# Kernel tuning notes

Hardware: AMD Instinct MI355X
Metric: run time of the kernel (lower is better)

## Reference

```python
import jax, jax.numpy as jnp
import numpy as np

D = 64        # emb_size
L = 4         # n_layers
ND = 4        # directions per layer: v2c, c2v, v2k, k2v
N_VAR, N_CONS, N_CUT = 100000, 50000, 20000
E_VC, E_VK = 800000, 200000
EF = 8        # edge feature dim
LN_EPS = 1e-3  # keras LayerNormalization default epsilon


def mlp2(x, w1, b1, w2, b2):
    # Dense(relu) -> Dense(linear); dropout is identity (training=False)
    return jax.nn.relu(x @ w1 + b1) @ w2 + b2


def layer_norm(x, g, b):
    m = jnp.mean(x, axis=-1, keepdims=True)
    v = jnp.var(x, axis=-1, keepdims=True)
    return (x - m) * jax.lax.rsqrt(v + LN_EPS) * g + b


def message_pass(node, neigh, src, dst, ew, P, i):
    """One MessagePassingLayer. P is a tuple of stacked [16,...] params, i the layer index."""
    (mw1, mb1, mw2, mb2, gw, gb, uw1, ub1, uw2, ub2, lg, lb) = P
    msg = mlp2(neigh, mw1[i], mb1[i], mw2[i], mb2[i])          # [N_src, D]
    wm = msg[src] * ew                                          # [E, D] gather + weight
    n = node.shape[0]
    agg = jax.ops.segment_sum(wm, dst, num_segments=n)          # scatter_nd sum
    deg = jax.ops.segment_sum(ew, dst, num_segments=n)          # [n, 1]
    agg = agg / jnp.maximum(deg, 1.0)
    comb = jnp.concatenate([agg, node], axis=-1)                # [n, 2D]
    gate = jax.nn.sigmoid(comb @ gw[i] + gb[i])
    upd = mlp2(comb, uw1[i], ub1[i], uw2[i], ub2[i])
    out = gate * upd + (1.0 - gate) * node
    return layer_norm(out, lg[i], lb[i])


def edge_weight(src_f, dst_f, e_f, w1, b1, w2, b2):
    comb = jnp.concatenate([src_f, dst_f, e_f], axis=-1)
    return jax.nn.sigmoid(jax.nn.relu(comb @ w1 + b1) @ w2 + b2)  # [E, 1]


def setup_inputs() -> dict:
    keys = iter(jax.random.split(jax.random.key(0), 64))

    def p(shape, scale=0.05):
        return jax.random.normal(next(keys), shape, dtype=jnp.float32) * scale

    inp = {
        'variable_features': jax.random.normal(next(keys), (N_VAR, 19), dtype=jnp.float32),
        'constraint_features': jax.random.normal(next(keys), (N_CONS, 5), dtype=jnp.float32),
        'cut_features': jax.random.normal(next(keys), (N_CUT, 30), dtype=jnp.float32),
        'var_cons_edge_features': jax.random.normal(next(keys), (E_VC, EF), dtype=jnp.float32),
        'var_cut_edge_features': jax.random.normal(next(keys), (E_VK, EF), dtype=jnp.float32),
        'var_cons_edges': jnp.stack([
            jax.random.randint(next(keys), (E_VC,), 0, N_VAR, dtype=jnp.int32),
            jax.random.randint(next(keys), (E_VC,), 0, N_CONS, dtype=jnp.int32)]),
        'var_cut_edges': jnp.stack([
            jax.random.randint(next(keys), (E_VK,), 0, N_VAR, dtype=jnp.int32),
            jax.random.randint(next(keys), (E_VK,), 0, N_CUT, dtype=jnp.int32)]),
    }
    # embedding MLPs
    for name, din in [('var', 19), ('cons', 5), ('cut', 30)]:
        inp[f'{name}_w1'] = p((din, D)); inp[f'{name}_b1'] = p((D,))
        inp[f'{name}_w2'] = p((D, D));  inp[f'{name}_b2'] = p((D,))
    # edge weight modules (input 2D + edge_feat)
    for name in ['ewvc', 'ewvk']:
        inp[f'{name}_w1'] = p((2 * D + EF, D)); inp[f'{name}_b1'] = p((D,))
        inp[f'{name}_w2'] = p((D, 1));          inp[f'{name}_b2'] = p((1,))
    # 16 message passing layers, stacked; index = layer*4 + direction(v2c,c2v,v2k,k2v)
    NL = L * ND
    inp['mp_msg_w1'] = p((NL, D, D));  inp['mp_msg_b1'] = p((NL, D))
    inp['mp_msg_w2'] = p((NL, D, D));  inp['mp_msg_b2'] = p((NL, D))
    inp['mp_gate_w'] = p((NL, 2 * D, D)); inp['mp_gate_b'] = p((NL, D))
    inp['mp_upd_w1'] = p((NL, 2 * D, D)); inp['mp_upd_b1'] = p((NL, D))
    inp['mp_upd_w2'] = p((NL, D, D));  inp['mp_upd_b2'] = p((NL, D))
    inp['mp_ln_g'] = jnp.ones((NL, D), dtype=jnp.float32)
    inp['mp_ln_b'] = jnp.zeros((NL, D), dtype=jnp.float32)
    return inp


def reference(variable_features, constraint_features, cut_features,
              var_cons_edge_features, var_cut_edge_features,
              var_w1, var_b1, var_w2, var_b2,
              cons_w1, cons_b1, cons_w2, cons_b2,
              cut_w1, cut_b1, cut_w2, cut_b2,
              ewvc_w1, ewvc_b1, ewvc_w2, ewvc_b2,
              ewvk_w1, ewvk_b1, ewvk_w2, ewvk_b2,
              mp_msg_w1, mp_msg_b1, mp_msg_w2, mp_msg_b2,
              mp_gate_w, mp_gate_b, mp_upd_w1, mp_upd_b1,
              mp_upd_w2, mp_upd_b2, mp_ln_g, mp_ln_b,
              var_cons_edges, var_cut_edges):
    h_var = mlp2(variable_features, var_w1, var_b1, var_w2, var_b2)
    h_cons = mlp2(constraint_features, cons_w1, cons_b1, cons_w2, cons_b2)
    h_cut = mlp2(cut_features, cut_w1, cut_b1, cut_w2, cut_b2)

    vc_s, vc_d = var_cons_edges[0], var_cons_edges[1]
    vk_s, vk_d = var_cut_edges[0], var_cut_edges[1]

    vc_w = edge_weight(h_var[vc_s], h_cons[vc_d], var_cons_edge_features,
                       ewvc_w1, ewvc_b1, ewvc_w2, ewvc_b2)
    vk_w = edge_weight(h_var[vk_s], h_cut[vk_d], var_cut_edge_features,
                       ewvk_w1, ewvk_b1, ewvk_w2, ewvk_b2)

    P = (mp_msg_w1, mp_msg_b1, mp_msg_w2, mp_msg_b2, mp_gate_w, mp_gate_b,
         mp_upd_w1, mp_upd_b1, mp_upd_w2, mp_upd_b2, mp_ln_g, mp_ln_b)

    for l in range(L):
        h_cons = message_pass(h_cons, h_var, vc_s, vc_d, vc_w, P, l * ND + 0)
        h_var = message_pass(h_var, h_cons, vc_d, vc_s, vc_w, P, l * ND + 1)  # reverse
        h_cut = message_pass(h_cut, h_var, vk_s, vk_d, vk_w, P, l * ND + 2)
        h_var = message_pass(h_var, h_cut, vk_d, vk_s, vk_w, P, l * ND + 3)  # reverse
    return h_cut
```

## Files before the change

### kernel.cpp

```cpp
#include <hip/hip_runtime.h>

#define DEVINL static __device__ __forceinline__

namespace {

typedef __attribute__((ext_vector_type(8))) short bf16x8;
typedef __attribute__((ext_vector_type(4))) float f32x4;

constexpr int NV = 100000;
constexpr int NC = 50000;
constexpr int NK = 20000;
constexpr int EVC = 800000;
constexpr int EVK = 200000;
constexpr int R_TOT = NC + NV + NK + NV;
constexpr int SCAN_CHUNK = 2048;
constexpr int SCAN_NB = (R_TOT + SCAN_CHUNK - 1) / SCAN_CHUNK;
constexpr int PACK_PER_LAYER = 28672;
constexpr float WQ_SCALE = 16383.0f;
constexpr float WQ_INV = 1.0f / 16383.0f;
constexpr int NBIN = 8;

constexpr int PE_VAR_W1 = 0;
constexpr int PE_VAR_W2 = 2048;
constexpr int PE_CONS_W1 = 6144;
constexpr int PE_CONS_W2 = 8192;
constexpr int PE_CUT_W1 = 12288;
constexpr int PE_CUT_W2 = 14336;
constexpr int PE_EWVC_A = 18432;
constexpr int PE_EWVC_B = 22528;
constexpr int PE_EWVK_A = 26624;
constexpr int PE_EWVK_B = 30720;
constexpr int PE_TOTAL = 34816;

DEVINL unsigned short f2bf(float f) {
  unsigned u = __float_as_uint(f);
  u = u + 0x7fffu + ((u >> 16) & 1u);
  return (unsigned short)(u >> 16);
}
DEVINL float bf2f(unsigned short h) {
  return __uint_as_float((unsigned)h << 16);
}

DEVINL float sigmoid_f(float x) { return 1.0f / (1.0f + __expf(-x)); }

DEVINL void pack_mat(const float* __restrict__ src, int K, int Kpad,
                     unsigned short* __restrict__ dst, int tid) {
  const int ntup = (Kpad / 32) * 256;
  for (int tup = tid; tup < ntup; tup += 256) {
    const int lane = tup & 63;
    const int t = (tup >> 6) & 3;
    const int kb = tup >> 8;
    const int c = t * 16 + (lane & 15);
    const int k0 = kb * 32 + (lane >> 4) * 8;
#pragma unroll
    for (int jj = 0; jj < 8; ++jj)
      dst[tup * 8 + jj] =
          (k0 + jj < K) ? f2bf(src[(k0 + jj) * 64 + c]) : (unsigned short)0;
  }
}

__global__ void __launch_bounds__(256) pack_k(
    const float* __restrict__ mW1, const float* __restrict__ mW2,
    const float* __restrict__ gW, const float* __restrict__ uW1,
    const float* __restrict__ uW2, unsigned short* __restrict__ PW) {
  const int layer = blockIdx.x;
  unsigned short* out = PW + (size_t)layer * PACK_PER_LAYER;
  pack_mat(mW1 + (size_t)layer * 4096, 64, 64, out, threadIdx.x);
  pack_mat(mW2 + (size_t)layer * 4096, 64, 64, out + 4096, threadIdx.x);
  pack_mat(gW + (size_t)layer * 8192, 128, 128, out + 8192, threadIdx.x);
  pack_mat(uW1 + (size_t)layer * 8192, 128, 128, out + 16384, threadIdx.x);
  pack_mat(uW2 + (size_t)layer * 4096, 64, 64, out + 24576, threadIdx.x);
}

__global__ void __launch_bounds__(256) pack_emb_k(
    const float* __restrict__ var_w1, const float* __restrict__ var_w2,
    const float* __restrict__ cons_w1, const float* __restrict__ cons_w2,
    const float* __restrict__ cut_w1, const float* __restrict__ cut_w2,
    const float* __restrict__ ewvc_w1, const float* __restrict__ ewvk_w1,
    unsigned short* __restrict__ P) {
  switch (blockIdx.x) {
    case 0: pack_mat(var_w1, 19, 32, P + PE_VAR_W1, threadIdx.x); break;
    case 1: pack_mat(var_w2, 64, 64, P + PE_VAR_W2, threadIdx.x); break;
    case 2: pack_mat(cons_w1, 5, 32, P + PE_CONS_W1, threadIdx.x); break;
    case 3: pack_mat(cons_w2, 64, 64, P + PE_CONS_W2, threadIdx.x); break;
    case 4: pack_mat(cut_w1, 30, 32, P + PE_CUT_W1, threadIdx.x); break;
    case 5: pack_mat(cut_w2, 64, 64, P + PE_CUT_W2, threadIdx.x); break;
    case 6: pack_mat(ewvc_w1, 64, 64, P + PE_EWVC_A, threadIdx.x); break;
    case 7: pack_mat(ewvc_w1 + 64 * 64, 64, 64, P + PE_EWVC_B, threadIdx.x); break;
    case 8: pack_mat(ewvk_w1, 64, 64, P + PE_EWVK_A, threadIdx.x); break;
    case 9: pack_mat(ewvk_w1 + 64 * 64, 64, 64, P + PE_EWVK_B, threadIdx.x); break;
  }
}

template <int DIN>
__global__ void __launch_bounds__(256) emb_mfma_k(
    const float* __restrict__ X, const unsigned short* __restrict__ W1p_,
    const unsigned short* __restrict__ W2p_, const float* __restrict__ B1,
    const float* __restrict__ B2, unsigned short* __restrict__ OUTb, int N) {
  __shared__ unsigned short lds[4][16 * 72];
  const int wave = threadIdx.x >> 6, l = threadIdx.x & 63;
  const int col = l & 15, quad = l >> 4;
  const int n0_raw = blockIdx.x * 64 + wave * 16;
  const bool dead = n0_raw >= N;
  const int n0 = dead ? 0 : n0_raw;

  bf16x8 a0;
#pragma unroll
  for (int j = 0; j < 8; ++j) {
    const int k = quad * 8 + j;
    a0[j] = (k < DIN) ? (short)f2bf(X[(size_t)(n0 + col) * DIN + k]) : (short)0;
  }
  const bf16x8* W1p = (const bf16x8*)W1p_;
  const bf16x8* W2p = (const bf16x8*)W2p_;
  f32x4 acc[4];
#pragma unroll
  for (int t = 0; t < 4; ++t) {
    const float b = B1[col + 16 * t];
    acc[t] = f32x4{b, b, b, b};
  }
#pragma unroll
  for (int t = 0; t < 4; ++t)
    acc[t] = __builtin_amdgcn_mfma_f32_16x16x32_bf16(a0, W1p[t * 64 + l], acc[t], 0, 0, 0);
  unsigned short* ld = lds[wave];
#pragma unroll
  for (int t = 0; t < 4; ++t)
#pragma unroll
    for (int r = 0; r < 4; ++r)
      ld[(quad * 4 + r) * 72 + col + 16 * t] = f2bf(fmaxf(acc[t][r], 0.0f));
  __syncthreads();
  const bf16x8 h0 = *(const bf16x8*)&ld[col * 72 + quad * 8];
  const bf16x8 h1 = *(const bf16x8*)&ld[col * 72 + 32 + quad * 8];
  f32x4 o[4];
#pragma unroll
  for (int t = 0; t < 4; ++t) {
    const float b = B2[col + 16 * t];
    o[t] = f32x4{b, b, b, b};
  }
#pragma unroll
  for (int t = 0; t < 4; ++t) {
    o[t] = __builtin_amdgcn_mfma_f32_16x16x32_bf16(h0, W2p[t * 64 + l], o[t], 0, 0, 0);
    o[t] = __builtin_amdgcn_mfma_f32_16x16x32_bf16(h1, W2p[(4 + t) * 64 + l], o[t], 0, 0, 0);
  }
  __syncthreads();
#pragma unroll
  for (int t = 0; t < 4; ++t)
#pragma unroll
    for (int r = 0; r < 4; ++r)
      ld[(quad * 4 + r) * 72 + col + 16 * t] = f2bf(o[t][r]);
  __syncthreads();
  if (!dead) {
#pragma unroll
    for (int cc = 0; cc < 2; ++cc) {
      const bf16x8 v = *(const bf16x8*)&ld[col * 72 + (quad * 2 + cc) * 8];
      *(bf16x8*)(OUTb + (size_t)(n0 + col) * 64 + (quad * 2 + cc) * 8) = v;
    }
  }
}

template <int NOUT>
__global__ void __launch_bounds__(256) gemv_mfma_k(
    const unsigned short* __restrict__ Xb, const unsigned short* __restrict__ WpA_,
    const unsigned short* __restrict__ WpB_, const float* __restrict__ Bias,
    unsigned short* __restrict__ OUT0, unsigned short* __restrict__ OUT1, int N) {
  __shared__ unsigned short lds[4][16 * 72];
  const int wave = threadIdx.x >> 6, l = threadIdx.x & 63;
  const int col = l & 15, quad = l >> 4;
  const int n0_raw = blockIdx.x * 64 + wave * 16;
  const bool dead = n0_raw >= N;
  const int n0 = dead ? 0 : n0_raw;
  const unsigned short* xrow = Xb + (size_t)(n0 + col) * 64 + quad * 8;
  const bf16x8 a0 = *(const bf16x8*)xrow;
  const bf16x8 a1 = *(const bf16x8*)(xrow + 32);
  unsigned short* ld = lds[wave];
#pragma unroll
  for (int m = 0; m < NOUT; ++m) {
    const bf16x8* Wp = (const bf16x8*)(m == 0 ? WpA_ : WpB_);
    unsigned short* OUT = (m == 0) ? OUT0 : OUT1;
    f32x4 acc[4];
#pragma unroll
    for (int t = 0; t < 4; ++t) {
      const float b = (Bias != nullptr) ? Bias[col + 16 * t] : 0.0f;
      acc[t] = f32x4{b, b, b, b};
    }
#pragma unroll
    for (int t = 0; t < 4; ++t) {
      acc[t] = __builtin_amdgcn_mfma_f32_16x16x32_bf16(a0, Wp[t * 64 + l], acc[t], 0, 0, 0);
      acc[t] = __builtin_amdgcn_mfma_f32_16x16x32_bf16(a1, Wp[(4 + t) * 64 + l], acc[t], 0, 0, 0);
    }
    if (m > 0) __syncthreads();
#pragma unroll
    for (int t = 0; t < 4; ++t)
#pragma unroll
      for (int r = 0; r < 4; ++r)
        ld[(quad * 4 + r) * 72 + col + 16 * t] = f2bf(acc[t][r]);
    __syncthreads();
    if (!dead) {
#pragma unroll
      for (int cc = 0; cc < 2; ++cc) {
        const bf16x8 v = *(const bf16x8*)&ld[col * 72 + (quad * 2 + cc) * 8];
        *(bf16x8*)(OUT + (size_t)(n0 + col) * 64 + (quad * 2 + cc) * 8) = v;
      }
    }
  }
}

__global__ void __launch_bounds__(256) msg_mfma_k(
    const unsigned short* __restrict__ Xb, const unsigned short* __restrict__ Wp,
    const float* __restrict__ B1, const float* __restrict__ B2,
    unsigned short* __restrict__ MSGb, int N) {
  __shared__ unsigned short lds[4][16 * 72];
  const int wave = threadIdx.x >> 6, l = threadIdx.x & 63;
  const int col = l & 15, quad = l >> 4;
  const int n0_raw = blockIdx.x * 64 + wave * 16;
  const bool dead = n0_raw >= N;
  const int n0 = dead ? 0 : n0_raw;

  const unsigned short* xrow = Xb + (size_t)(n0 + col) * 64 + quad * 8;
  const bf16x8 a0 = *(const bf16x8*)xrow;
  const bf16x8 a1 = *(const bf16x8*)(xrow + 32);
  const bf16x8* W1p = (const bf16x8*)Wp;
  const bf16x8* W2p = (const bf16x8*)(Wp + 4096);

  f32x4 acc[4];
#pragma unroll
  for (int t = 0; t < 4; ++t) {
    const float b = B1[col + 16 * t];
    acc[t] = f32x4{b, b, b, b};
  }
#pragma unroll
  for (int t = 0; t < 4; ++t) {
    acc[t] = __builtin_amdgcn_mfma_f32_16x16x32_bf16(a0, W1p[t * 64 + l], acc[t], 0, 0, 0);
    acc[t] = __builtin_amdgcn_mfma_f32_16x16x32_bf16(a1, W1p[(4 + t) * 64 + l], acc[t], 0, 0, 0);
  }
  unsigned short* ld = lds[wave];
#pragma unroll
  for (int t = 0; t < 4; ++t)
#pragma unroll
    for (int r = 0; r < 4; ++r)
      ld[(quad * 4 + r) * 72 + col + 16 * t] = f2bf(fmaxf(acc[t][r], 0.0f));
  __syncthreads();
  const bf16x8 h0 = *(const bf16x8*)&ld[col * 72 + quad * 8];
  const bf16x8 h1 = *(const bf16x8*)&ld[col * 72 + 32 + quad * 8];
  f32x4 o[4];
#pragma unroll
  for (int t = 0; t < 4; ++t) {
    const float b = B2[col + 16 * t];
    o[t] = f32x4{b, b, b, b};
  }
#pragma unroll
  for (int t = 0; t < 4; ++t) {
    o[t] = __builtin_amdgcn_mfma_f32_16x16x32_bf16(h0, W2p[t * 64 + l], o[t], 0, 0, 0);
    o[t] = __builtin_amdgcn_mfma_f32_16x16x32_bf16(h1, W2p[(4 + t) * 64 + l], o[t], 0, 0, 0);
  }
  __syncthreads();
#pragma unroll
  for (int t = 0; t < 4; ++t)
#pragma unroll
    for (int r = 0; r < 4; ++r)
      ld[(quad * 4 + r) * 72 + col + 16 * t] = f2bf(o[t][r]);
  __syncthreads();
  if (!dead) {
#pragma unroll
    for (int cc = 0; cc < 2; ++cc) {
      const bf16x8 v = *(const bf16x8*)&ld[col * 72 + (quad * 2 + cc) * 8];
      *(bf16x8*)(MSGb + (size_t)(n0 + col) * 64 + (quad * 2 + cc) * 8) = v;
    }
  }
}

template <int WITH_MSG>
__global__ void __launch_bounds__(256) pass_mfma_k(
    const int* __restrict__ row_ptr, const unsigned* __restrict__ adj,
    const float* __restrict__ degi, const unsigned short* __restrict__ MSGsrc,
    const unsigned short* __restrict__ NODEb,
    const unsigned short* __restrict__ gWp, const unsigned short* __restrict__ uW1p,
    const unsigned short* __restrict__ uW2p, const float* __restrict__ gB,
    const float* __restrict__ uB1, const float* __restrict__ uB2,
    const float* __restrict__ LNG, const float* __restrict__ LNB,
    const unsigned short* __restrict__ mWp,
    const float* __restrict__ mB1, const float* __restrict__ mB2,
    float* __restrict__ OUTf, unsigned short* __restrict__ OUTb,
    unsigned short* __restrict__ MSGdst, int base, int N) {
  __shared__ unsigned short lds[4][16 * 72];
  const int wave = threadIdx.x >> 6, l = threadIdx.x & 63;
  const int col = l & 15, quad = l >> 4;
  const int n0_raw = blockIdx.x * 64 + wave * 16;
  const bool dead = n0_raw >= N;
  const int n0 = dead ? 0 : n0_raw;

  const int r = base + n0 + col;
  const int ps = row_ptr[r], pe = row_ptr[r + 1];
  float acc0[8], acc1[8];
#pragma unroll
  for (int j = 0; j < 8; ++j) { acc0[j] = 0.0f; acc1[j] = 0.0f; }
  int p = ps;
  for (; p + 2 <= pe; p += 2) {
    const unsigned avA = adj[p], avB = adj[p + 1];
    const unsigned short* mA = MSGsrc + (size_t)(avA >> 14) * 64 + quad * 8;
    const unsigned short* mB = MSGsrc + (size_t)(avB >> 14) * 64 + quad * 8;
    const bf16x8 mA0 = *(const bf16x8*)mA;
    const bf16x8 mA1 = *(const bf16x8*)(mA + 32);
    const bf16x8 mB0 = *(const bf16x8*)mB;
    const bf16x8 mB1v = *(const bf16x8*)(mB + 32);
    const float wA = (float)(avA & 16383u) * WQ_INV;
    const float wB = (float)(avB & 16383u) * WQ_INV;
    const unsigned* uA0 = (const unsigned*)&mA0;
    const unsigned* uA1 = (const unsigned*)&mA1;
    const unsigned* uB0 = (const unsigned*)&mB0;
    const unsigned* uB1v = (const unsigned*)&mB1v;
#pragma unroll
    for (int q = 0; q < 4; ++q) {
      acc0[2 * q] = fmaf(__uint_as_float(uA0[q] << 16), wA, acc0[2 * q]);
      acc0[2 * q + 1] = fmaf(__uint_as_float(uA0[q] & 0xffff0000u), wA, acc0[2 * q + 1]);
      acc1[2 * q] = fmaf(__uint_as_float(uA1[q] << 16), wA, acc1[2 * q]);
      acc1[2 * q + 1] = fmaf(__uint_as_float(uA1[q] & 0xffff0000u), wA, acc1[2 * q + 1]);
      acc0[2 * q] = fmaf(__uint_as_float(uB0[q] << 16), wB, acc0[2 * q]);
      acc0[2 * q + 1] = fmaf(__uint_as_float(uB0[q] & 0xffff0000u), wB, acc0[2 * q + 1]);
      acc1[2 * q] = fmaf(__uint_as_float(uB1v[q] << 16), wB, acc1[2 * q]);
      acc1[2 * q + 1] = fmaf(__uint_as_float(uB1v[q] & 0xffff0000u), wB, acc1[2 * q + 1]);
    }
  }
  if (p < pe) {
    const unsigned av = adj[p];
    const unsigned short* m = MSGsrc + (size_t)(av >> 14) * 64 + quad * 8;
    const bf16x8 m0 = *(const bf16x8*)m;
    const bf16x8 m1 = *(const bf16x8*)(m + 32);
    const float w = (float)(av & 16383u) * WQ_INV;
    const unsigned* u0 = (const unsigned*)&m0;
    const unsigned* u1 = (const unsigned*)&m1;
#pragma unroll
    for (int q = 0; q < 4; ++q) {
      acc0[2 * q] = fmaf(__uint_as_float(u0[q] << 16), w, acc0[2 * q]);
      acc0[2 * q + 1] = fmaf(__uint_as_float(u0[q] & 0xffff0000u), w, acc0[2 * q + 1]);
      acc1[2 * q] = fmaf(__uint_as_float(u1[q] << 16), w, acc1[2 * q]);
      acc1[2 * q + 1] = fmaf(__uint_as_float(u1[q] & 0xffff0000u), w, acc1[2 * q + 1]);
    }
  }
  const float di = degi[r];
  bf16x8 aA0, aA1;
#pragma unroll
  for (int j = 0; j < 8; ++j) {
    aA0[j] = (short)f2bf(acc0[j] * di);
    aA1[j] = (short)f2bf(acc1[j] * di);
  }

  const unsigned short* nrow = NODEb + (size_t)(n0 + col) * 64 + quad * 8;
  const bf16x8 aN0 = *(const bf16x8*)nrow;
  const bf16x8 aN1 = *(const bf16x8*)(nrow + 32);
  const bf16x8* gW = (const bf16x8*)gWp;
  const bf16x8* uW1 = (const bf16x8*)uW1p;
  const bf16x8* uW2 = (const bf16x8*)uW2p;

  f32x4 g[4], u[4];
#pragma unroll
  for (int t = 0; t < 4; ++t) {
    const float bg = gB[col + 16 * t], bu = uB1[col + 16 * t];
    g[t] = f32x4{bg, bg, bg, bg};
    u[t] = f32x4{bu, bu, bu, bu};
  }
#pragma unroll
  for (int t = 0; t < 4; ++t) {
    g[t] = __builtin_amdgcn_mfma_f32_16x16x32_bf16(aA0, gW[t * 64 + l], g[t], 0, 0, 0);
    g[t] = __builtin_amdgcn_mfma_f32_16x16x32_bf16(aA1, gW[(4 + t) * 64 + l], g[t], 0, 0, 0);
    g[t] = __builtin_amdgcn_mfma_f32_16x16x32_bf16(aN0, gW[(8 + t) * 64 + l], g[t], 0, 0, 0);
    g[t] = __builtin_amdgcn_mfma_f32_16x16x32_bf16(aN1, gW[(12 + t) * 64 + l], g[t], 0, 0, 0);
    u[t] = __builtin_amdgcn_mfma_f32_16x16x32_bf16(aA0, uW1[t * 64 + l], u[t], 0, 0, 0);
    u[t] = __builtin_amdgcn_mfma_f32_16x16x32_bf16(aA1, uW1[(4 + t) * 64 + l], u[t], 0, 0, 0);
    u[t] = __builtin_amdgcn_mfma_f32_16x16x32_bf16(aN0, uW1[(8 + t) * 64 + l], u[t], 0, 0, 0);
    u[t] = __builtin_amdgcn_mfma_f32_16x16x32_bf16(aN1, uW1[(12 + t) * 64 + l], u[t], 0, 0, 0);
  }
#pragma unroll
  for (int t = 0; t < 4; ++t)
#pragma unroll
    for (int r2 = 0; r2 < 4; ++r2) g[t][r2] = sigmoid_f(g[t][r2]);

  unsigned short* ld = lds[wave];
#pragma unroll
  for (int t = 0; t < 4; ++t)
#pragma unroll
    for (int r2 = 0; r2 < 4; ++r2)
      ld[(quad * 4 + r2) * 72 + col + 16 * t] = f2bf(fmaxf(u[t][r2], 0.0f));
  __syncthreads();
  const bf16x8 h0 = *(const bf16x8*)&ld[col * 72 + quad * 8];
  const bf16x8 h1 = *(const bf16x8*)&ld[col * 72 + 32 + quad * 8];
  f32x4 o[4];
#pragma unroll
  for (int t = 0; t < 4; ++t) {
    const float b = uB2[col + 16 * t];
    o[t] = f32x4{b, b, b, b};
  }
#pragma unroll
  for (int t = 0; t < 4; ++t) {
    o[t] = __builtin_amdgcn_mfma_f32_16x16x32_bf16(h0, uW2[t * 64 + l], o[t], 0, 0, 0);
    o[t] = __builtin_amdgcn_mfma_f32_16x16x32_bf16(h1, uW2[(4 + t) * 64 + l], o[t], 0, 0, 0);
  }
  float om[4][4];
#pragma unroll
  for (int t = 0; t < 4; ++t)
#pragma unroll
    for (int r2 = 0; r2 < 4; ++r2) {
      const float nd =
          bf2f(NODEb[(size_t)(n0 + quad * 4 + r2) * 64 + col + 16 * t]);
      om[t][r2] = fmaf(g[t][r2], o[t][r2] - nd, nd);
    }
  float outv[4][4];
#pragma unroll
  for (int r2 = 0; r2 < 4; ++r2) {
    float s1 = (om[0][r2] + om[1][r2]) + (om[2][r2] + om[3][r2]);
    float s2 = fmaf(om[0][r2], om[0][r2], fmaf(om[1][r2], om[1][r2],
                fmaf(om[2][r2], om[2][r2], om[3][r2] * om[3][r2])));
#pragma unroll
    for (int off = 1; off < 16; off <<= 1) {
      s1 += __shfl_xor(s1, off, 64);
      s2 += __shfl_xor(s2, off, 64);
    }
    const float m = s1 * (1.0f / 64.0f);
    const float var = s2 * (1.0f / 64.0f) - m * m;
    const float rr = rsqrtf(var + 1e-3f);
#pragma unroll
    for (int t = 0; t < 4; ++t)
      outv[t][r2] = fmaf((om[t][r2] - m) * rr, LNG[col + 16 * t], LNB[col + 16 * t]);
  }
  if (OUTf != nullptr && !dead) {
#pragma unroll
    for (int t = 0; t < 4; ++t)
#pragma unroll
      for (int r2 = 0; r2 < 4; ++r2)
        OUTf[(size_t)(n0 + quad * 4 + r2) * 64 + col + 16 * t] = outv[t][r2];
  }
  __syncthreads();
#pragma unroll
  for (int t = 0; t < 4; ++t)
#pragma unroll
    for (int r2 = 0; r2 < 4; ++r2)
      ld[(quad * 4 + r2) * 72 + col + 16 * t] = f2bf(outv[t][r2]);
  __syncthreads();
  if (OUTb != nullptr && !dead) {
#pragma unroll
    for (int cc = 0; cc < 2; ++cc) {
      const bf16x8 v = *(const bf16x8*)&ld[col * 72 + (quad * 2 + cc) * 8];
      *(bf16x8*)(OUTb + (size_t)(n0 + col) * 64 + (quad * 2 + cc) * 8) = v;
    }
  }

  if constexpr (WITH_MSG) {
    const bf16x8 x0 = *(const bf16x8*)&ld[col * 72 + quad * 8];
    const bf16x8 x1 = *(const bf16x8*)&ld[col * 72 + 32 + quad * 8];
    const bf16x8* W1p = (const bf16x8*)mWp;
    const bf16x8* W2p = (const bf16x8*)(mWp + 4096);
    f32x4 macc[4];
#pragma unroll
    for (int t = 0; t < 4; ++t) {
      const float b = mB1[col + 16 * t];
      macc[t] = f32x4{b, b, b, b};
    }
#pragma unroll
    for (int t = 0; t < 4; ++t) {
      macc[t] = __builtin_amdgcn_mfma_f32_16x16x32_bf16(x0, W1p[t * 64 + l], macc[t], 0, 0, 0);
      macc[t] = __builtin_amdgcn_mfma_f32_16x16x32_bf16(x1, W1p[(4 + t) * 64 + l], macc[t], 0, 0, 0);
    }
    __syncthreads();
#pragma unroll
    for (int t = 0; t < 4; ++t)
#pragma unroll
      for (int r2 = 0; r2 < 4; ++r2)
        ld[(quad * 4 + r2) * 72 + col + 16 * t] = f2bf(fmaxf(macc[t][r2], 0.0f));
    __syncthreads();
    const bf16x8 mh0 = *(const bf16x8*)&ld[col * 72 + quad * 8];
    const bf16x8 mh1 = *(const bf16x8*)&ld[col * 72 + 32 + quad * 8];
    f32x4 mo[4];
#pragma unroll
    for (int t = 0; t < 4; ++t) {
      const float b = mB2[col + 16 * t];
      mo[t] = f32x4{b, b, b, b};
    }
#pragma unroll
    for (int t = 0; t < 4; ++t) {
      mo[t] = __builtin_amdgcn_mfma_f32_16x16x32_bf16(mh0, W2p[t * 64 + l], mo[t], 0, 0, 0);
      mo[t] = __builtin_amdgcn_mfma_f32_16x16x32_bf16(mh1, W2p[(4 + t) * 64 + l], mo[t], 0, 0, 0);
    }
    __syncthreads();
#pragma unroll
    for (int t = 0; t < 4; ++t)
#pragma unroll
      for (int r2 = 0; r2 < 4; ++r2)
        ld[(quad * 4 + r2) * 72 + col + 16 * t] = f2bf(mo[t][r2]);
    __syncthreads();
    if (!dead) {
#pragma unroll
      for (int cc = 0; cc < 2; ++cc) {
        const bf16x8 v = *(const bf16x8*)&ld[col * 72 + (quad * 2 + cc) * 8];
        *(bf16x8*)(MSGdst + (size_t)(n0 + col) * 64 + (quad * 2 + cc) * 8) = v;
      }
    }
  }
}

__global__ void __launch_bounds__(256) edgew_k(
    const int* __restrict__ S, const int* __restrict__ D,
    const float* __restrict__ EFX, const unsigned short* __restrict__ PA,
    const unsigned short* __restrict__ PB, const float* __restrict__ W1C,
    const float* __restrict__ W2, const float* __restrict__ B2,
    float* __restrict__ EW, int* __restrict__ counts, int baseD, int baseS,
    int E) {
  const int l = threadIdx.x & 63;
  const int g = l >> 3, c = l & 7;
  float wc[8][8];
#pragma unroll
  for (int i = 0; i < 8; ++i) {
    const float4 v0 = *(const float4*)(W1C + i * 64 + c * 8);
    const float4 v1 = *(const float4*)(W1C + i * 64 + c * 8 + 4);
    wc[i][0] = v0.x; wc[i][1] = v0.y; wc[i][2] = v0.z; wc[i][3] = v0.w;
    wc[i][4] = v1.x; wc[i][5] = v1.y; wc[i][6] = v1.z; wc[i][7] = v1.w;
  }
  float w2c[8];
  {
    const float4 a0 = *(const float4*)(W2 + c * 8);
    const float4 a1 = *(const float4*)(W2 + c * 8 + 4);
    w2c[0] = a0.x; w2c[1] = a0.y; w2c[2] = a0.z; w2c[3] = a0.w;
    w2c[4] = a1.x; w2c[5] = a1.y; w2c[6] = a1.z; w2c[7] = a1.w;
  }
  const float b2 = B2[0];
  const int wave_id = blockIdx.x * 4 + (threadIdx.x >> 6);
  const int nwaves = gridDim.x * 4;
  for (int t0 = wave_id * 8; t0 < E; t0 += nwaves * 8) {
    const int e = t0 + g;
    const bool ok = e < E;
    const int ee = ok ? e : E - 1;
    const int s = __builtin_nontemporal_load(S + ee);
    const int d = __builtin_nontemporal_load(D + ee);
    const bf16x8 pa = *(const bf16x8*)(PA + (size_t)s * 64 + c * 8);
    const bf16x8 pb = *(const bf16x8*)(PB + (size_t)d * 64 + c * 8);
    const f32x4 ef0 =
        __builtin_nontemporal_load((const f32x4*)(EFX + (size_t)ee * 8));
    const f32x4 ef1 =
        __builtin_nontemporal_load((const f32x4*)(EFX + (size_t)ee * 8 + 4));
    const unsigned* pau = (const unsigned*)&pa;
    const unsigned* pbu = (const unsigned*)&pb;
    float h[8];
#pragma unroll
    for (int q = 0; q < 4; ++q) {
      h[2 * q] = __uint_as_float(pau[q] << 16) + __uint_as_float(pbu[q] << 16);
      h[2 * q + 1] = __uint_as_float(pau[q] & 0xffff0000u) +
                     __uint_as_float(pbu[q] & 0xffff0000u);
    }
    const float ef[8] = {ef0[0], ef0[1], ef0[2], ef0[3],
                         ef1[0], ef1[1], ef1[2], ef1[3]};
#pragma unroll
    for (int i = 0; i < 8; ++i)
#pragma unroll
      for (int j = 0; j < 8; ++j) h[j] = fmaf(ef[i], wc[i][j], h[j]);
    float t = 0.0f;
#pragma unroll
    for (int j = 0; j < 8; ++j) t = fmaf(fmaxf(h[j], 0.0f), w2c[j], t);
#pragma unroll
    for (int off = 1; off < 8; off <<= 1) t += __shfl_xor(t, off, 64);
    if (ok && c == 0) {
      EW[e] = sigmoid_f(t + b2);
      atomicAdd(&counts[baseD + d], 1);
      atomicAdd(&counts[baseS + s], 1);
    }
  }
}

__global__ void __launch_bounds__(256) fill_binned_k(
    const int* __restrict__ S, const int* __restrict__ D,
    const float* __restrict__ EW, int* __restrict__ cursor,
    unsigned* __restrict__ adj, int baseD, int baseS, int NDrows, int NSrows,
    int E) {
  const int bin = blockIdx.x & (NBIN - 1);
  const int blk = blockIdx.x / NBIN;
  const int nblk = gridDim.x / NBIN;
  const int d_lo = (int)((long long)NDrows * bin / NBIN);
  const int d_hi = (int)((long long)NDrows * (bin + 1) / NBIN);
  const int s_lo = (int)((long long)NSrows * bin / NBIN);
  const int s_hi = (int)((long long)NSrows * (bin + 1) / NBIN);
  for (int e = blk * 256 + threadIdx.x; e < E; e += nblk * 256) {
    const int s = __builtin_nontemporal_load(S + e);
    const int d = __builtin_nontemporal_load(D + e);
    const bool md = (d >= d_lo) & (d < d_hi);
    const bool ms = (s >= s_lo) & (s < s_hi);
    if (md | ms) {
      const float w = __builtin_nontemporal_load(EW + e);
      const unsigned w14 = (unsigned)(w * WQ_SCALE + 0.5f);
      if (md) {
        const int p = atomicAdd(&cursor[baseD + d], 1);
        adj[p] = ((unsigned)s << 14) | w14;
      }
      if (ms) {
        const int p = atomicAdd(&cursor[baseS + s], 1);
        adj[p] = ((unsigned)d << 14) | w14;
      }
    }
  }
}

__global__ void __launch_bounds__(256) degi_k(const int* __restrict__ row_ptr,
                                             const unsigned* __restrict__ adj,
                                             float* __restrict__ degi) {
  const int r = blockIdx.x * 256 + threadIdx.x;
  if (r >= R_TOT) return;
  const int s = row_ptr[r], e = row_ptr[r + 1];
  float d = 0.0f;
  for (int p = s; p < e; ++p) d += (float)(adj[p] & 16383u) * WQ_INV;
  degi[r] = 1.0f / fmaxf(d, 1.0f);
}

__global__ void __launch_bounds__(256) scan1_k(const int* __restrict__ in,
                                               int* __restrict__ bsum) {
  __shared__ int sd[256];
  const int t = threadIdx.x;
  const int base = blockIdx.x * SCAN_CHUNK + t * 8;
  int s = 0;
#pragma unroll
  for (int i = 0; i < 8; ++i) {
    const int idx = base + i;
    s += (idx < R_TOT) ? in[idx] : 0;
  }
  sd[t] = s;
  __syncthreads();
  for (int off = 128; off > 0; off >>= 1) {
    if (t < off) sd[t] += sd[t + off];
    __syncthreads();
  }
  if (t == 0) bsum[blockIdx.x] = sd[0];
}

__global__ void __launch_bounds__(256) scan2_k(int* __restrict__ bsum,
                                               int* __restrict__ row_ptr) {
  __shared__ int sd[256];
  const int t = threadIdx.x;
  const int v = (t < SCAN_NB) ? bsum[t] : 0;
  sd[t] = v;
  __syncthreads();
  for (int off = 1; off < 256; off <<= 1) {
    const int add = (t >= off) ? sd[t - off] : 0;
    __syncthreads();
    sd[t] += add;
    __syncthreads();
  }
  if (t < SCAN_NB) bsum[t] = sd[t] - v;
  if (t == 255) row_ptr[R_TOT] = sd[255];
}

__global__ void __launch_bounds__(256) scan3_k(const int* __restrict__ in,
                                               const int* __restrict__ bsum,
                                               int* __restrict__ out) {
  __shared__ int sd[256];
  const int t = threadIdx.x;
  const int base = blockIdx.x * SCAN_CHUNK + t * 8;
  int loc[8];
  int s = 0;
#pragma unroll
  for (int i = 0; i < 8; ++i) {
    loc[i] = s;
    const int idx = base + i;
    s += (idx < R_TOT) ? in[idx] : 0;
  }
  sd[t] = s;
  __syncthreads();
  const int v = s;
  for (int off = 1; off < 256; off <<= 1) {
    const int add = (t >= off) ? sd[t - off] : 0;
    __syncthreads();
    sd[t] += add;
    __syncthreads();
  }
  const int off0 = bsum[blockIdx.x] + (sd[t] - v);
#pragma unroll
  for (int i = 0; i < 8; ++i) {
    const int idx = base + i;
    if (idx < R_TOT) out[idx] = off0 + loc[i];
  }
}

}

extern "C" void kernel_launch(void* const* d_in, const int* in_sizes, int n_in,
                              void* d_out, int out_size, void* d_ws, size_t ws_size,
                              hipStream_t stream) {
  (void)in_sizes; (void)n_in; (void)out_size; (void)ws_size;

  const float* variable_features   = (const float*)d_in[0];
  const float* constraint_features = (const float*)d_in[1];
  const float* cut_features        = (const float*)d_in[2];
  const float* vc_ef = (const float*)d_in[3];
  const float* vk_ef = (const float*)d_in[4];
  const int* vc_edges = (const int*)d_in[5];
  const int* vk_edges = (const int*)d_in[6];
  const int *vc_s = vc_edges, *vc_d = vc_edges + EVC;
  const int *vk_s = vk_edges, *vk_d = vk_edges + EVK;
  const float* var_w1  = (const float*)d_in[7];
  const float* var_b1  = (const float*)d_in[8];
  const float* var_w2  = (const float*)d_in[9];
  const float* var_b2  = (const float*)d_in[10];
  const float* cons_w1 = (const float*)d_in[11];
  const float* cons_b1 = (const float*)d_in[12];
  const float* cons_w2 = (const float*)d_in[13];
  const float* cons_b2 = (const float*)d_in[14];
  const float* cut_w1  = (const float*)d_in[15];
  const float* cut_b1  = (const float*)d_in[16];
  const float* cut_w2  = (const float*)d_in[17];
  const float* cut_b2  = (const float*)d_in[18];
  const float* ewvc_w1 = (const float*)d_in[19];
  const float* ewvc_b1 = (const float*)d_in[20];
  const float* ewvc_w2 = (const float*)d_in[21];
  const float* ewvc_b2 = (const float*)d_in[22];
  const float* ewvk_w1 = (const float*)d_in[23];
  const float* ewvk_b1 = (const float*)d_in[24];
  const float* ewvk_w2 = (const float*)d_in[25];
  const float* ewvk_b2 = (const float*)d_in[26];
  const float* mp_msg_w1 = (const float*)d_in[27];
  const float* mp_msg_b1 = (const float*)d_in[28];
  const float* mp_msg_w2 = (const float*)d_in[29];
  const float* mp_msg_b2 = (const float*)d_in[30];
  const float* mp_gate_w = (const float*)d_in[31];
  const float* mp_gate_b = (const float*)d_in[32];
  const float* mp_upd_w1 = (const float*)d_in[33];
  const float* mp_upd_b1 = (const float*)d_in[34];
  const float* mp_upd_w2 = (const float*)d_in[35];
  const float* mp_upd_b2 = (const float*)d_in[36];
  const float* mp_ln_g   = (const float*)d_in[37];
  const float* mp_ln_b   = (const float*)d_in[38];

  char* wp = (char*)d_ws;
  auto take = [&](size_t nbytes) {
    char* p = wp;
    wp += (nbytes + 255) & ~(size_t)255;
    return p;
  };
  unsigned short* h_var_b  = (unsigned short*)take((size_t)NV * 64 * 2);
  unsigned short* h_cons_b = (unsigned short*)take((size_t)NC * 64 * 2);
  unsigned short* h_cut_b  = (unsigned short*)take((size_t)NK * 64 * 2);
  unsigned short* msg_ping = (unsigned short*)take((size_t)NV * 64 * 2);
  unsigned short* msg_pong = (unsigned short*)take((size_t)NV * 64 * 2);
  unsigned short* pa = (unsigned short*)take((size_t)NV * 64 * 2);
  unsigned short* pb = (unsigned short*)take((size_t)NC * 64 * 2);
  unsigned short* qa = (unsigned short*)take((size_t)NV * 64 * 2);
  unsigned short* qb = (unsigned short*)take((size_t)NK * 64 * 2);
  unsigned short* packW = (unsigned short*)take((size_t)15 * PACK_PER_LAYER * 2);
  unsigned short* packE = (unsigned short*)take((size_t)PE_TOTAL * 2);
  float* ew_vc = (float*)take((size_t)EVC * 4);
  float* ew_vk = (float*)take((size_t)EVK * 4);
  int* row_ptr = (int*)take((size_t)(R_TOT + 1) * 4);
  int* cursor  = (int*)take((size_t)R_TOT * 4);
  int* counts  = (int*)take((size_t)R_TOT * 4);
  int* bsum    = (int*)take(256 * 4);
  float* degi  = (float*)take((size_t)R_TOT * 4);
  unsigned* adj = (unsigned*)take((size_t)(2 * EVC + 2 * EVK) * 4);

  hipMemsetAsync(counts, 0, (size_t)R_TOT * 4, stream);

  pack_k<<<15, 256, 0, stream>>>(mp_msg_w1, mp_msg_w2, mp_gate_w, mp_upd_w1,
                                 mp_upd_w2, packW);
  pack_emb_k<<<10, 256, 0, stream>>>(var_w1, var_w2, cons_w1, cons_w2, cut_w1,
                                     cut_w2, ewvc_w1, ewvk_w1, packE);

  emb_mfma_k<19><<<(NV + 63) / 64, 256, 0, stream>>>(
      variable_features, packE + PE_VAR_W1, packE + PE_VAR_W2, var_b1, var_b2,
      h_var_b, NV);
  emb_mfma_k<5><<<(NC + 63) / 64, 256, 0, stream>>>(
      constraint_features, packE + PE_CONS_W1, packE + PE_CONS_W2, cons_b1,
      cons_b2, h_cons_b, NC);
  emb_mfma_k<30><<<(NK + 63) / 64, 256, 0, stream>>>(
      cut_features, packE + PE_CUT_W1, packE + PE_CUT_W2, cut_b1, cut_b2,
      h_cut_b, NK);

  gemv_mfma_k<2><<<(NV + 63) / 64, 256, 0, stream>>>(
      h_var_b, packE + PE_EWVC_A, packE + PE_EWVK_A, nullptr, pa, qa, NV);
  gemv_mfma_k<1><<<(NC + 63) / 64, 256, 0, stream>>>(
      h_cons_b, packE + PE_EWVC_B, nullptr, ewvc_b1, pb, nullptr, NC);
  gemv_mfma_k<1><<<(NK + 63) / 64, 256, 0, stream>>>(
      h_cut_b, packE + PE_EWVK_B, nullptr, ewvk_b1, qb, nullptr, NK);

  edgew_k<<<1024, 256, 0, stream>>>(vc_s, vc_d, vc_ef, pa, pb,
                                    ewvc_w1 + 128 * 64, ewvc_w2, ewvc_b2,
                                    ew_vc, counts, 0, NC, EVC);
  edgew_k<<<512, 256, 0, stream>>>(vk_s, vk_d, vk_ef, qa, qb,
                                   ewvk_w1 + 128 * 64, ewvk_w2, ewvk_b2,
                                   ew_vk, counts, NC + NV, NC + NV + NK, EVK);

  scan1_k<<<SCAN_NB, 256, 0, stream>>>(counts, bsum);
  scan2_k<<<1, 256, 0, stream>>>(bsum, row_ptr);
  scan3_k<<<SCAN_NB, 256, 0, stream>>>(counts, bsum, row_ptr);
  hipMemcpyAsync(cursor, row_ptr, (size_t)R_TOT * 4, hipMemcpyDeviceToDevice, stream);
  fill_binned_k<<<NBIN * 128, 256, 0, stream>>>(vc_s, vc_d, ew_vc, cursor, adj,
                                                0, NC, NC, NV, EVC);
  fill_binned_k<<<NBIN * 64, 256, 0, stream>>>(vk_s, vk_d, ew_vk, cursor, adj,
                                               NC + NV, NC + NV + NK, NK, NV, EVK);
  degi_k<<<(R_TOT + 255) / 256, 256, 0, stream>>>(row_ptr, adj, degi);

  unsigned short* nodeb_t[4] = {h_cons_b, h_var_b, h_cut_b, h_var_b};
  const int Nd_t[4] = {NC, NV, NK, NV};
  const int base_t[4] = {0, NC, NC + NV, NC + NV + NK};

  msg_mfma_k<<<(NV + 63) / 64, 256, 0, stream>>>(
      h_var_b, packW, mp_msg_b1, mp_msg_b2, msg_ping, NV);

  for (int i = 0; i < 15; ++i) {
    const int d = i & 3;
    const int Nd = Nd_t[d], base = base_t[d];
    const unsigned short* Wl = packW + (size_t)i * PACK_PER_LAYER;
    const unsigned short* src = (i % 2 == 0) ? msg_ping : msg_pong;
    unsigned short* dst = (i % 2 == 0) ? msg_pong : msg_ping;

    if (i < 14) {
      const unsigned short* Wn = packW + (size_t)(i + 1) * PACK_PER_LAYER;
      pass_mfma_k<1><<<(Nd + 63) / 64, 256, 0, stream>>>(
          row_ptr, adj, degi, src, nodeb_t[d], Wl + 8192, Wl + 16384,
          Wl + 24576, mp_gate_b + (size_t)i * 64, mp_upd_b1 + (size_t)i * 64,
          mp_upd_b2 + (size_t)i * 64, mp_ln_g + (size_t)i * 64,
          mp_ln_b + (size_t)i * 64, Wn, mp_msg_b1 + (size_t)(i + 1) * 64,
          mp_msg_b2 + (size_t)(i + 1) * 64, nullptr, nodeb_t[d], dst, base, Nd);
    } else {
      pass_mfma_k<0><<<(Nd + 63) / 64, 256, 0, stream>>>(
          row_ptr, adj, degi, src, nodeb_t[d], Wl + 8192, Wl + 16384,
          Wl + 24576, mp_gate_b + (size_t)i * 64, mp_upd_b1 + (size_t)i * 64,
          mp_upd_b2 + (size_t)i * 64, mp_ln_g + (size_t)i * 64,
          mp_ln_b + (size_t)i * 64, nullptr, nullptr, nullptr,
          (float*)d_out, nullptr, nullptr, base, Nd);
    }
  }
}
```

Baseline: 926.2 us.

## Stage binned adjacency entries in edge-weight kernel, replacing fill pass with scatter

The edge-weight kernel now quantizes each weight and bins the (row, packed value) pairs for both directions into eight row-range bins. It buffers them in shared memory and flushes them in chunks to global staging arrays. A new scatter kernel then reads each bin and places entries through the per-row cursor. This drops the per-edge float weight array and the fill_binned pass, which re-read src/dst/weights once per bin. The cost is extra block-wide syncs per iteration, a large 64-bit staging buffer, and fixed bin capacities that assume the given edge distribution.

```diff
diff --git a/kernel.cpp b/kernel.cpp
--- a/kernel.cpp
+++ b/kernel.cpp
@@ -18,7 +18,10 @@
 constexpr int PACK_PER_LAYER = 28672;
 constexpr float WQ_SCALE = 16383.0f;
 constexpr float WQ_INV = 1.0f / 16383.0f;
-constexpr int NBIN = 8;
+
+constexpr int ROW_BIN_HI[8] = {15625, 31250, 46875, 75000,
+                               106250, 137500, 165000, 270000};
+constexpr int BIN_CAP = 294912;
 
 constexpr int PE_VAR_W1 = 0;
 constexpr int PE_VAR_W2 = 2048;
@@ -42,6 +45,13 @@
 }
 
 DEVINL float sigmoid_f(float x) { return 1.0f / (1.0f + __expf(-x)); }
+
+DEVINL int row_bin(int r) {
+  int b = 0;
+#pragma unroll
+  for (int i = 0; i < 7; ++i) b += (r >= ROW_BIN_HI[i]);
+  return b;
+}
 
 DEVINL void pack_mat(const float* __restrict__ src, int K, int Kpad,
                      unsigned short* __restrict__ dst, int tid) {
@@ -501,9 +511,12 @@
     const float* __restrict__ EFX, const unsigned short* __restrict__ PA,
     const unsigned short* __restrict__ PB, const float* __restrict__ W1C,
     const float* __restrict__ W2, const float* __restrict__ B2,
-    float* __restrict__ EW, int* __restrict__ counts, int baseD, int baseS,
-    int E) {
+    int* __restrict__ counts, int* __restrict__ bcur,
+    unsigned long long* __restrict__ staged, int baseD, int baseS, int E) {
+  __shared__ unsigned long long sbuf[8][128];
+  __shared__ int scnt[8];
   const int l = threadIdx.x & 63;
+  const int wave = threadIdx.x >> 6;
   const int g = l >> 3, c = l & 7;
   float wc[8][8];
 #pragma unroll
@@ -521,10 +534,11 @@
     w2c[4] = a1.x; w2c[5] = a1.y; w2c[6] = a1.z; w2c[7] = a1.w;
   }
   const float b2 = B2[0];
-  const int wave_id = blockIdx.x * 4 + (threadIdx.x >> 6);
-  const int nwaves = gridDim.x * 4;
-  for (int t0 = wave_id * 8; t0 < E; t0 += nwaves * 8) {
-    const int e = t0 + g;
+  if (threadIdx.x < 8) scnt[threadIdx.x] = 0;
+  __syncthreads();
+
+  for (int tb = blockIdx.x * 32; tb < E; tb += gridDim.x * 32) {
+    const int e = tb + wave * 8 + g;
     const bool ok = e < E;
     const int ee = ok ? e : E - 1;
     const int s = __builtin_nontemporal_load(S + ee);
@@ -555,43 +569,67 @@
     for (int j = 0; j < 8; ++j) t = fmaf(fmaxf(h[j], 0.0f), w2c[j], t);
 #pragma unroll
     for (int off = 1; off < 8; off <<= 1) t += __shfl_xor(t, off, 64);
+
     if (ok && c == 0) {
-      EW[e] = sigmoid_f(t + b2);
+      const float w = sigmoid_f(t + b2);
+      const unsigned w14 = (unsigned)(w * WQ_SCALE + 0.5f);
       atomicAdd(&counts[baseD + d], 1);
       atomicAdd(&counts[baseS + s], 1);
-    }
-  }
-}
-
-__global__ void __launch_bounds__(256) fill_binned_k(
-    const int* __restrict__ S, const int* __restrict__ D,
-    const float* __restrict__ EW, int* __restrict__ cursor,
-    unsigned* __restrict__ adj, int baseD, int baseS, int NDrows, int NSrows,
-    int E) {
-  const int bin = blockIdx.x & (NBIN - 1);
-  const int blk = blockIdx.x / NBIN;
-  const int nblk = gridDim.x / NBIN;
-  const int d_lo = (int)((long long)NDrows * bin / NBIN);
-  const int d_hi = (int)((long long)NDrows * (bin + 1) / NBIN);
-  const int s_lo = (int)((long long)NSrows * bin / NBIN);
-  const int s_hi = (int)((long long)NSrows * (bin + 1) / NBIN);
-  for (int e = blk * 256 + threadIdx.x; e < E; e += nblk * 256) {
-    const int s = __builtin_nontemporal_load(S + e);
-    const int d = __builtin_nontemporal_load(D + e);
-    const bool md = (d >= d_lo) & (d < d_hi);
-    const bool ms = (s >= s_lo) & (s < s_hi);
-    if (md | ms) {
-      const float w = __builtin_nontemporal_load(EW + e);
-      const unsigned w14 = (unsigned)(w * WQ_SCALE + 0.5f);
-      if (md) {
-        const int p = atomicAdd(&cursor[baseD + d], 1);
-        adj[p] = ((unsigned)s << 14) | w14;
+      const int rd = baseD + d;
+      const int bd = row_bin(rd);
+      int pos = atomicAdd(&scnt[bd], 1);
+      sbuf[bd][pos] = (unsigned long long)(unsigned)rd |
+                      ((unsigned long long)(((unsigned)s << 14) | w14) << 32);
+      const int rs = baseS + s;
+      const int bs = row_bin(rs);
+      pos = atomicAdd(&scnt[bs], 1);
+      sbuf[bs][pos] = (unsigned long long)(unsigned)rs |
+                      ((unsigned long long)(((unsigned)d << 14) | w14) << 32);
+    }
+    __syncthreads();
+#pragma unroll
+    for (int bi = 0; bi < 2; ++bi) {
+      const int bb = wave * 2 + bi;
+      const int cnt = scnt[bb];
+      if (cnt >= 64) {
+        int sb = 0;
+        if (l == 0) sb = atomicAdd(&bcur[bb], cnt);
+        sb = __shfl(sb, 0);
+        for (int i = l; i < cnt; i += 64)
+          staged[(size_t)bb * BIN_CAP + sb + i] = sbuf[bb][i];
+        if (l == 0) scnt[bb] = 0;
       }
-      if (ms) {
-        const int p = atomicAdd(&cursor[baseS + s], 1);
-        adj[p] = ((unsigned)d << 14) | w14;
-      }
-    }
+    }
+    __syncthreads();
+  }
+#pragma unroll
+  for (int bi = 0; bi < 2; ++bi) {
+    const int bb = wave * 2 + bi;
+    const int cnt = scnt[bb];
+    if (cnt > 0) {
+      int sb = 0;
+      if (l == 0) sb = atomicAdd(&bcur[bb], cnt);
+      sb = __shfl(sb, 0);
+      for (int i = l; i < cnt; i += 64)
+        staged[(size_t)bb * BIN_CAP + sb + i] = sbuf[bb][i];
+    }
+  }
+}
+
+__global__ void __launch_bounds__(256) scatter_k(
+    const unsigned long long* __restrict__ staged, const int* __restrict__ bcur,
+    int* __restrict__ cursor, unsigned* __restrict__ adj) {
+  const int bin = blockIdx.x & 7;
+  const int blk = blockIdx.x >> 3;
+  const int nblk = gridDim.x >> 3;
+  const int n = bcur[bin];
+  const unsigned long long* src = staged + (size_t)bin * BIN_CAP;
+  for (int i = blk * 256 + threadIdx.x; i < n; i += nblk * 256) {
+    const unsigned long long v = __builtin_nontemporal_load(src + i);
+    const int row = (int)(unsigned)(v & 0xffffffffull);
+    const unsigned val = (unsigned)(v >> 32);
+    const int p = atomicAdd(&cursor[row], 1);
+    adj[p] = val;
   }
 }
 
@@ -740,8 +778,9 @@
   unsigned short* qb = (unsigned short*)take((size_t)NK * 64 * 2);
   unsigned short* packW = (unsigned short*)take((size_t)15 * PACK_PER_LAYER * 2);
   unsigned short* packE = (unsigned short*)take((size_t)PE_TOTAL * 2);
-  float* ew_vc = (float*)take((size_t)EVC * 4);
-  float* ew_vk = (float*)take((size_t)EVK * 4);
+  unsigned long long* staged =
+      (unsigned long long*)take((size_t)8 * BIN_CAP * 8);
+  int* bcur = (int*)take(8 * 4);
   int* row_ptr = (int*)take((size_t)(R_TOT + 1) * 4);
   int* cursor  = (int*)take((size_t)R_TOT * 4);
   int* counts  = (int*)take((size_t)R_TOT * 4);
@@ -750,6 +789,7 @@
   unsigned* adj = (unsigned*)take((size_t)(2 * EVC + 2 * EVK) * 4);
 
   hipMemsetAsync(counts, 0, (size_t)R_TOT * 4, stream);
+  hipMemsetAsync(bcur, 0, 8 * 4, stream);
 
   pack_k<<<15, 256, 0, stream>>>(mp_msg_w1, mp_msg_w2, mp_gate_w, mp_upd_w1,
                                  mp_upd_w2, packW);
@@ -775,19 +815,17 @@
 
   edgew_k<<<1024, 256, 0, stream>>>(vc_s, vc_d, vc_ef, pa, pb,
                                     ewvc_w1 + 128 * 64, ewvc_w2, ewvc_b2,
-                                    ew_vc, counts, 0, NC, EVC);
+                                    counts, bcur, staged, 0, NC, EVC);
   edgew_k<<<512, 256, 0, stream>>>(vk_s, vk_d, vk_ef, qa, qb,
                                    ewvk_w1 + 128 * 64, ewvk_w2, ewvk_b2,
-                                   ew_vk, counts, NC + NV, NC + NV + NK, EVK);
+                                   counts, bcur, staged, NC + NV,
+                                   NC + NV + NK, EVK);
 
   scan1_k<<<SCAN_NB, 256, 0, stream>>>(counts, bsum);
   scan2_k<<<1, 256, 0, stream>>>(bsum, row_ptr);
   scan3_k<<<SCAN_NB, 256, 0, stream>>>(counts, bsum, row_ptr);
   hipMemcpyAsync(cursor, row_ptr, (size_t)R_TOT * 4, hipMemcpyDeviceToDevice, stream);
-  fill_binned_k<<<NBIN * 128, 256, 0, stream>>>(vc_s, vc_d, ew_vc, cursor, adj,
-                                                0, NC, NC, NV, EVC);
-  fill_binned_k<<<NBIN * 64, 256, 0, stream>>>(vk_s, vk_d, ew_vk, cursor, adj,
-                                               NC + NV, NC + NV + NK, NK, NV, EVK);
+  scatter_k<<<8 * 128, 256, 0, stream>>>(staged, bcur, cursor, adj);
   degi_k<<<(R_TOT + 255) / 256, 256, 0, stream>>>(row_ptr, adj, degi);
 
   unsigned short* nodeb_t[4] = {h_cons_b, h_var_b, h_cut_b, h_var_b};
```

Measured after the change: 1.200 ms. 1.3x slower.

## Reserve adjacency slots in edge-weight kernel and fill CSR from staged records

Applied to the files above, without the earlier changes.

The edge-weight kernel now takes each edge's per-row slot index from the counting atomics and writes packed 64-bit records (row, slot, neighbour, quantised weight) to a staging buffer that reuses the message ping/pong space. A single binned fill kernel then scatters these records into the adjacency array at row_ptr + slot, with no atomics. This removes the cursor copy, the second round of atomics and the re-reads of S, D and EW in the old fill kernels. In exchange, 16 MB of staged records are written and read back. The packing also caps per-row degree at 8191 and row count at 2^19, and the staging runs past msg_ping into msg_pong.

```diff
diff --git a/kernel.cpp b/kernel.cpp
--- a/kernel.cpp
+++ b/kernel.cpp
@@ -12,13 +12,21 @@
 constexpr int NK = 20000;
 constexpr int EVC = 800000;
 constexpr int EVK = 200000;
+constexpr int E_TOT2 = 2 * (EVC + EVK);
 constexpr int R_TOT = NC + NV + NK + NV;
 constexpr int SCAN_CHUNK = 2048;
 constexpr int SCAN_NB = (R_TOT + SCAN_CHUNK - 1) / SCAN_CHUNK;
 constexpr int PACK_PER_LAYER = 28672;
 constexpr float WQ_SCALE = 16383.0f;
 constexpr float WQ_INV = 1.0f / 16383.0f;
-constexpr int NBIN = 8;
+
+constexpr int ROW_BIN_HI[8] = {12500, 25000, 37500, 50000,
+                               83334, 116667, 150000, 270000};
+__constant__ int c_bin_hi[8] = {12500, 25000, 37500, 50000,
+                                83334, 116667, 150000, 270000};
+__constant__ int c_seg_lo[8] = {0, 0, 0, 0, EVC, EVC, EVC, 2 * EVC};
+__constant__ int c_seg_hi[8] = {EVC, EVC, EVC, EVC,
+                                2 * EVC, 2 * EVC, 2 * EVC, E_TOT2};
 
 constexpr int PE_VAR_W1 = 0;
 constexpr int PE_VAR_W2 = 2048;
@@ -501,8 +509,9 @@
     const float* __restrict__ EFX, const unsigned short* __restrict__ PA,
     const unsigned short* __restrict__ PB, const float* __restrict__ W1C,
     const float* __restrict__ W2, const float* __restrict__ B2,
-    float* __restrict__ EW, int* __restrict__ counts, int baseD, int baseS,
-    int E) {
+    unsigned long long* __restrict__ stagedD,
+    unsigned long long* __restrict__ stagedS,
+    int* __restrict__ counts, int baseD, int baseS, int E) {
   const int l = threadIdx.x & 63;
   const int g = l >> 3, c = l & 7;
   float wc[8][8];
@@ -529,6 +538,12 @@
     const int ee = ok ? e : E - 1;
     const int s = __builtin_nontemporal_load(S + ee);
     const int d = __builtin_nontemporal_load(D + ee);
+    int kd = 0, ks = 0;
+    const int rd = baseD + d, rs = baseS + s;
+    if (ok && c == 0) {
+      kd = atomicAdd(&counts[rd], 1);
+      ks = atomicAdd(&counts[rs], 1);
+    }
     const bf16x8 pa = *(const bf16x8*)(PA + (size_t)s * 64 + c * 8);
     const bf16x8 pb = *(const bf16x8*)(PB + (size_t)d * 64 + c * 8);
     const f32x4 ef0 =
@@ -556,41 +571,33 @@
 #pragma unroll
     for (int off = 1; off < 8; off <<= 1) t += __shfl_xor(t, off, 64);
     if (ok && c == 0) {
-      EW[e] = sigmoid_f(t + b2);
-      atomicAdd(&counts[baseD + d], 1);
-      atomicAdd(&counts[baseS + s], 1);
-    }
-  }
-}
-
-__global__ void __launch_bounds__(256) fill_binned_k(
-    const int* __restrict__ S, const int* __restrict__ D,
-    const float* __restrict__ EW, int* __restrict__ cursor,
-    unsigned* __restrict__ adj, int baseD, int baseS, int NDrows, int NSrows,
-    int E) {
-  const int bin = blockIdx.x & (NBIN - 1);
-  const int blk = blockIdx.x / NBIN;
-  const int nblk = gridDim.x / NBIN;
-  const int d_lo = (int)((long long)NDrows * bin / NBIN);
-  const int d_hi = (int)((long long)NDrows * (bin + 1) / NBIN);
-  const int s_lo = (int)((long long)NSrows * bin / NBIN);
-  const int s_hi = (int)((long long)NSrows * (bin + 1) / NBIN);
-  for (int e = blk * 256 + threadIdx.x; e < E; e += nblk * 256) {
-    const int s = __builtin_nontemporal_load(S + e);
-    const int d = __builtin_nontemporal_load(D + e);
-    const bool md = (d >= d_lo) & (d < d_hi);
-    const bool ms = (s >= s_lo) & (s < s_hi);
-    if (md | ms) {
-      const float w = __builtin_nontemporal_load(EW + e);
+      const float w = sigmoid_f(t + b2);
       const unsigned w14 = (unsigned)(w * WQ_SCALE + 0.5f);
-      if (md) {
-        const int p = atomicAdd(&cursor[baseD + d], 1);
-        adj[p] = ((unsigned)s << 14) | w14;
-      }
-      if (ms) {
-        const int p = atomicAdd(&cursor[baseS + s], 1);
-        adj[p] = ((unsigned)d << 14) | w14;
-      }
+      stagedD[e] =
+          (unsigned long long)((unsigned)rd | ((unsigned)kd << 19)) |
+          ((unsigned long long)(((unsigned)s << 14) | w14) << 32);
+      stagedS[e] =
+          (unsigned long long)((unsigned)rs | ((unsigned)ks << 19)) |
+          ((unsigned long long)(((unsigned)d << 14) | w14) << 32);
+    }
+  }
+}
+
+__global__ void __launch_bounds__(256) fill_staged_k(
+    const unsigned long long* __restrict__ staged,
+    const int* __restrict__ row_ptr, unsigned* __restrict__ adj) {
+  const int bin = blockIdx.x & 7;
+  const int blk = blockIdx.x >> 3;
+  const int nblk = gridDim.x >> 3;
+  const int lo = (bin == 0) ? 0 : c_bin_hi[bin - 1];
+  const int hi = c_bin_hi[bin];
+  const int slo = c_seg_lo[bin], shi = c_seg_hi[bin];
+  for (int i = slo + blk * 256 + threadIdx.x; i < shi; i += nblk * 256) {
+    const unsigned long long v = __builtin_nontemporal_load(staged + i);
+    const int row = (int)(v & 0x7ffffull);
+    if (row >= lo && row < hi) {
+      const int k = (int)((v >> 19) & 0x1fffull);
+      adj[row_ptr[row] + k] = (unsigned)(v >> 32);
     }
   }
 }
@@ -740,14 +747,13 @@
   unsigned short* qb = (unsigned short*)take((size_t)NK * 64 * 2);
   unsigned short* packW = (unsigned short*)take((size_t)15 * PACK_PER_LAYER * 2);
   unsigned short* packE = (unsigned short*)take((size_t)PE_TOTAL * 2);
-  float* ew_vc = (float*)take((size_t)EVC * 4);
-  float* ew_vk = (float*)take((size_t)EVK * 4);
   int* row_ptr = (int*)take((size_t)(R_TOT + 1) * 4);
-  int* cursor  = (int*)take((size_t)R_TOT * 4);
   int* counts  = (int*)take((size_t)R_TOT * 4);
   int* bsum    = (int*)take(256 * 4);
   float* degi  = (float*)take((size_t)R_TOT * 4);
   unsigned* adj = (unsigned*)take((size_t)(2 * EVC + 2 * EVK) * 4);
+
+  unsigned long long* staged = (unsigned long long*)msg_ping;
 
   hipMemsetAsync(counts, 0, (size_t)R_TOT * 4, stream);
 
@@ -775,19 +781,16 @@
 
   edgew_k<<<1024, 256, 0, stream>>>(vc_s, vc_d, vc_ef, pa, pb,
                                     ewvc_w1 + 128 * 64, ewvc_w2, ewvc_b2,
-                                    ew_vc, counts, 0, NC, EVC);
+                                    staged, staged + EVC, counts, 0, NC, EVC);
   edgew_k<<<512, 256, 0, stream>>>(vk_s, vk_d, vk_ef, qa, qb,
                                    ewvk_w1 + 128 * 64, ewvk_w2, ewvk_b2,
-                                   ew_vk, counts, NC + NV, NC + NV + NK, EVK);
+                                   staged + 2 * EVC, staged + 2 * EVC + EVK,
+                                   counts, NC + NV, NC + NV + NK, EVK);
 
   scan1_k<<<SCAN_NB, 256, 0, stream>>>(counts, bsum);
   scan2_k<<<1, 256, 0, stream>>>(bsum, row_ptr);
   scan3_k<<<SCAN_NB, 256, 0, stream>>>(counts, bsum, row_ptr);
-  hipMemcpyAsync(cursor, row_ptr, (size_t)R_TOT * 4, hipMemcpyDeviceToDevice, stream);
-  fill_binned_k<<<NBIN * 128, 256, 0, stream>>>(vc_s, vc_d, ew_vc, cursor, adj,
-                                                0, NC, NC, NV, EVC);
-  fill_binned_k<<<NBIN * 64, 256, 0, stream>>>(vk_s, vk_d, ew_vk, cursor, adj,
-                                               NC + NV, NC + NV + NK, NK, NV, EVK);
+  fill_staged_k<<<8 * 192, 256, 0, stream>>>(staged, row_ptr, adj);
   degi_k<<<(R_TOT + 255) / 256, 256, 0, stream>>>(row_ptr, adj, degi);
 
   unsigned short* nodeb_t[4] = {h_cons_b, h_var_b, h_cut_b, h_var_b};
```

New measurement: 837.4 us. 1.11x faster.
